# Kernel tuning notes

Hardware: AMD Instinct MI355X
Metric: run time of the kernel (lower is better)

Reference implementation:

```python
import jax, jax.numpy as jnp
import numpy as np

N_HEADS = 8
N_LAYERS = 2
LN_EPS = 1e-5


def _mha(x, Win, bin_, Wout, bout):
    # torch nn.MultiheadAttention, eval mode (dropout off). x: [b, s, d]
    b, s, d = x.shape
    dh = d // N_HEADS
    qkv = x @ Win.T + bin_                      # [b, s, 3d]
    q, k, v = jnp.split(qkv, 3, axis=-1)
    q = q.reshape(b, s, N_HEADS, dh)
    k = k.reshape(b, s, N_HEADS, dh)
    v = v.reshape(b, s, N_HEADS, dh)
    scores = jnp.einsum('bqhd,bkhd->bhqk', q, k) / jnp.sqrt(jnp.asarray(dh, x.dtype))
    attn = jax.nn.softmax(scores, axis=-1)
    o = jnp.einsum('bhqk,bkhd->bqhd', attn, v).reshape(b, s, d)
    return o @ Wout.T + bout


def _layer_norm(x, g, b):
    mu = jnp.mean(x, axis=-1, keepdims=True)
    var = jnp.mean(jnp.square(x - mu), axis=-1, keepdims=True)
    return (x - mu) * jax.lax.rsqrt(var + LN_EPS) * g + b


def _vertex_conv(feat, inc, prev, Win, bin_, Wout, bout, Wproj, ln_g, ln_b, alpha):
    # feat: [b,m,d], inc: [b,m,e]
    attn = _mha(feat, Win, bin_, Wout, bout)              # [b,m,d]
    scores = jnp.einsum('bme,bmd->bed', inc, attn)        # incidence aggregation
    w = jax.nn.softmax(scores, axis=1)                    # softmax over edges
    # fused form of einsum('bme,bmd->bmed') then einsum('bmed,bed->bed')
    edge = scores * w                                     # [b,e,d]
    edge = edge @ Wproj.T                                 # no-bias projection
    edge = _layer_norm(edge, ln_g, ln_b)
    if prev is not None:
        edge = alpha * prev + (1.0 - alpha) * edge
        edge = edge + prev
    return edge


def _edge_conv(inc, edge_feat, prev, Win, bin_, Wout, bout, Wproj, ln_g, ln_b, alpha):
    # inc: [b,m,e], edge_feat: [b,e,d]
    _ = _mha(edge_feat, Win, bin_, Wout, bout)            # attn computed, output unused downstream
    wef = jnp.einsum('bed,bme->bmd', edge_feat, inc)      # edge->node aggregation
    node = wef @ Wproj.T
    node = _layer_norm(node, ln_g, ln_b)
    if prev is not None:
        node = alpha * prev + (1.0 - alpha) * node
        node = node + prev
    return node


def setup_inputs() -> dict:
    key = jax.random.key(0)
    ks = jax.random.split(key, 8)
    b, m, e, d = 8, 1024, 1536, 256
    s = 0.02
    return {
        'features': jax.random.normal(ks[0], (b, m, d), jnp.float32),
        'inc_mat': (jax.random.uniform(ks[1], (b, m, e), jnp.float32) < 0.05).astype(jnp.float32),
        'vc_Win': jax.random.normal(ks[2], (3 * d, d), jnp.float32) * s,
        'vc_bin': jnp.zeros((3 * d,), jnp.float32),
        'vc_Wout': jax.random.normal(ks[3], (d, d), jnp.float32) * s,
        'vc_bout': jnp.zeros((d,), jnp.float32),
        'vc_Wproj': jax.random.normal(ks[4], (d, d), jnp.float32) * s,
        'vc_ln_g': jnp.ones((d,), jnp.float32),
        'vc_ln_b': jnp.zeros((d,), jnp.float32),
        'vc_alpha': jnp.asarray(0.5, jnp.float32),
        'ec_Win': jax.random.normal(ks[5], (3 * d, d), jnp.float32) * s,
        'ec_bin': jnp.zeros((3 * d,), jnp.float32),
        'ec_Wout': jax.random.normal(ks[6], (d, d), jnp.float32) * s,
        'ec_bout': jnp.zeros((d,), jnp.float32),
        'ec_Wproj': jax.random.normal(ks[7], (d, d), jnp.float32) * s,
        'ec_ln_g': jnp.ones((d,), jnp.float32),
        'ec_ln_b': jnp.zeros((d,), jnp.float32),
        'ec_alpha': jnp.asarray(0.5, jnp.float32),
    }


def reference(features, inc_mat,
              vc_Win, vc_bin, vc_Wout, vc_bout, vc_Wproj, vc_ln_g, vc_ln_b, vc_alpha,
              ec_Win, ec_bin, ec_Wout, ec_bout, ec_Wproj, ec_ln_g, ec_ln_b, ec_alpha):
    vc = (vc_Win, vc_bin, vc_Wout, vc_bout, vc_Wproj, vc_ln_g, vc_ln_b, vc_alpha)
    ec = (ec_Win, ec_bin, ec_Wout, ec_bout, ec_Wproj, ec_ln_g, ec_ln_b, ec_alpha)
    edge_feats = _vertex_conv(features, inc_mat, None, *vc)
    node_feats = _edge_conv(inc_mat, edge_feats, features, *ec)
    for _ in range(N_LAYERS):  # shared weights across layers, as in the torch module
        edge_feats = _vertex_conv(features, inc_mat, edge_feats, *vc)
        node_feats = _edge_conv(inc_mat, edge_feats, node_feats, *ec)
    return node_feats, edge_feats, inc_mat
```

## Files before the change

### kernel.cpp

```cpp
#include <hip/hip_runtime.h>
#include <stdint.h>


#define DEV static __device__ __forceinline__

typedef __attribute__((ext_vector_type(8))) short bf16x8;
typedef __attribute__((ext_vector_type(4))) float f32x4;

DEV uint16_t f2bf(float x){
  union{float f; uint32_t u;} v; v.f=x;
  uint32_t r = v.u + 0x7fffu + ((v.u>>16)&1u);
  return (uint16_t)(r>>16);
}
DEV float bf2f(uint16_t b){
  union{uint32_t u; float f;} v; v.u=((uint32_t)b)<<16; return v.f;
}

DEV uint32_t cvtpk_bf16(float lo, float hi){
  uint32_t d;
  asm("v_cvt_pk_bf16_f32 %0, %1, %2" : "=v"(d) : "v"(lo), "v"(hi));
  return d;
}

#if __has_builtin(__builtin_amdgcn_exp2f)
DEV float exp2fast(float x){ return __builtin_amdgcn_exp2f(x); }
#else
DEV float exp2fast(float x){ return __expf(x * 0.6931471805599453f); }
#endif

#if __has_builtin(__builtin_amdgcn_global_load_lds)
#define HAVE_GLL 1
#else
#define HAVE_GLL 0
#endif

DEV void load_lds16(const uint16_t* g, void* l){
#if HAVE_GLL
  __builtin_amdgcn_global_load_lds((const __attribute__((address_space(1))) uint32_t*)g,
                                   (__attribute__((address_space(3))) uint32_t*)l, 16, 0, 0);
#else
  *(bf16x8*)l = *(const bf16x8*)g;
#endif
}

__global__ __launch_bounds__(256)
void prep_cast(const float* __restrict__ feats, const float* __restrict__ win,
               const float* __restrict__ wout, const float* __restrict__ wpv,
               const float* __restrict__ wpe,
               uint16_t* __restrict__ xb, uint16_t* __restrict__ ow,
               uint16_t* __restrict__ oo, uint16_t* __restrict__ ov,
               uint16_t* __restrict__ oe){
  int i = blockIdx.x*256 + threadIdx.x;
  const float* src; uint16_t* dst; int j;
  if (i < 524288){ src=feats; dst=xb; j=i; }
  else {
    i -= 524288;
    if (i < 49152){ src=win; dst=ow; j=i; }
    else if (i < 65536){ src=wout; dst=oo; j=i-49152; }
    else if (i < 81920){ src=wpv; dst=ov; j=i-65536; }
    else { src=wpe; dst=oe; j=i-81920; }
  }
  float4 v = ((const float4*)src)[j];
  union { uint16_t u[4]; uint64_t q; } p;
  p.u[0]=f2bf(v.x); p.u[1]=f2bf(v.y); p.u[2]=f2bf(v.z); p.u[3]=f2bf(v.w);
  ((uint64_t*)dst)[j] = p.q;
}

__global__ __launch_bounds__(256, 3)
void qkv_incprep(const float* __restrict__ inc, float* __restrict__ out_inc,
                 uint16_t* __restrict__ incb, uint16_t* __restrict__ incT,
                 const uint16_t* __restrict__ A, const uint16_t* __restrict__ B,
                 uint16_t* __restrict__ Cb, const float* __restrict__ bias){
  __shared__ union {
    struct { short As[128*64]; short Bs[128*64]; } g;
    float T[32][33];
  } sm;
  const int tid = threadIdx.x;
  const int bx = blockIdx.x;

  if (bx < 384){
    const int lane = tid & 63;
    const int w = tid >> 6;
    const int wm = w & 1, wn = w >> 1;
    const int r = lane & 15, q = lane >> 4;
    const int mtile = bx & 63, ntile = bx >> 6;
    const uint16_t* Ab = A + (size_t)(mtile*128)*256;
    const uint16_t* Bb = B + (size_t)(ntile*128)*256;
    f32x4 acc[4][4];
#pragma unroll
    for (int i=0;i<4;++i)
#pragma unroll
      for (int j=0;j<4;++j) acc[i][j] = (f32x4){0.f,0.f,0.f,0.f};

    const int srow = tid >> 3;
    const int sblk = tid & 7;

    for (int kb = 0; kb < 256; kb += 64){
#pragma unroll
      for (int i=0;i<4;++i){
        int row = srow + 32*i;
        int lblk = sblk ^ (row & 7);
        load_lds16(Ab + (size_t)row*256 + kb + lblk*8, (char*)sm.g.As + i*4096 + tid*16);
      }
#pragma unroll
      for (int i=0;i<4;++i){
        int row = srow + 32*i;
        int lblk = sblk ^ (row & 7);
        load_lds16(Bb + (size_t)row*256 + kb + lblk*8, (char*)sm.g.Bs + i*4096 + tid*16);
      }
      __syncthreads();
#pragma unroll
      for (int kc=0;kc<2;++kc){
        bf16x8 af[4], bfr[4];
#pragma unroll
        for (int mt=0;mt<4;++mt){
          int m = wm*64 + mt*16 + r;
          af[mt] = *(const bf16x8*)&sm.g.As[m*64 + ((kc*4 + q) ^ (m&7))*8];
        }
#pragma unroll
        for (int nt=0;nt<4;++nt){
          int n = wn*64 + nt*16 + r;
          bfr[nt] = *(const bf16x8*)&sm.g.Bs[n*64 + ((kc*4 + q) ^ (n&7))*8];
        }
#pragma unroll
        for (int mt=0;mt<4;++mt)
#pragma unroll
          for (int nt=0;nt<4;++nt)
            acc[mt][nt] = __builtin_amdgcn_mfma_f32_16x16x32_bf16(af[mt], bfr[nt], acc[mt][nt], 0,0,0);
      }
      __syncthreads();
    }

    const int gm0 = mtile*128 + wm*64;
    const int gn0 = ntile*128 + wn*64;
#pragma unroll
    for (int mt=0;mt<4;++mt){
#pragma unroll
      for (int nt=0;nt<4;++nt){
        int gn = gn0 + nt*16 + r;
        float bv = bias[gn];
#pragma unroll
        for (int reg=0;reg<4;++reg){
          int gm = gm0 + mt*16 + q*4 + reg;
          Cb[(size_t)gm*768 + gn] = f2bf(acc[mt][nt][reg] + bv);
        }
      }
    }
  } else {
    int bxp = bx - 384;
    int x = bxp % 48;
    int t = bxp / 48;
    int y = t % 32;
    int b = t / 32;
    int c0 = x*32, r0 = y*32;
    int tx = tid & 31, ty = tid >> 5;
    size_t base = (size_t)b*1024*1536;
#pragma unroll
    for (int j=0;j<4;++j){
      int r = r0 + ty + j*8;
      size_t idx = base + (size_t)r*1536 + c0 + tx;
      float v = inc[idx];
      sm.T[ty+j*8][tx] = v;
      out_inc[idx] = v;
      incb[idx] = f2bf(v);
    }
    __syncthreads();
    size_t baseT = (size_t)b*1536*1024;
#pragma unroll
    for (int j=0;j<4;++j){
      int c = c0 + ty + j*8;
      incT[baseT + (size_t)c*1024 + r0 + tx] = f2bf(sm.T[tx][ty+j*8]);
    }
  }
}

template<int WM, int BK, int EPI>
__global__ __launch_bounds__(256, 3)
void gemm_nt(const uint16_t* __restrict__ A, const uint16_t* __restrict__ B,
             uint16_t* __restrict__ Cb, const float* __restrict__ bias,
             int M, int N, int K){
  constexpr int AROWS = WM*32;
  constexpr int UPR = BK/8;
  constexpr int RPP = 256/UPR;
  __shared__ short As[AROWS*BK];
  __shared__ short Bs[128*BK];
  const int tid = threadIdx.x;
  const int lane = tid & 63;
  const int w = tid >> 6;
  const int wm = w & 1, wn = w >> 1;
  const int r = lane & 15, q = lane >> 4;
  const uint16_t* Ab = A + (size_t)(blockIdx.x*AROWS)*K;
  const uint16_t* Bb = B + (size_t)(blockIdx.y*128)*K;
  f32x4 acc[WM][4];
#pragma unroll
  for (int i=0;i<WM;++i)
#pragma unroll
    for (int j=0;j<4;++j) acc[i][j] = (f32x4){0.f,0.f,0.f,0.f};

  const int srow = tid / UPR;
  const int sblk = tid % UPR;

  for (int kb = 0; kb < K; kb += BK){
#pragma unroll
    for (int i=0;i<AROWS/RPP;++i){
      int row = srow + RPP*i;
      int lblk = sblk ^ (row & (UPR-1));
      load_lds16(Ab + (size_t)row*K + kb + lblk*8, (char*)As + i*4096 + tid*16);
    }
#pragma unroll
    for (int i=0;i<128/RPP;++i){
      int row = srow + RPP*i;
      int lblk = sblk ^ (row & (UPR-1));
      load_lds16(Bb + (size_t)row*K + kb + lblk*8, (char*)Bs + i*4096 + tid*16);
    }
    __syncthreads();
#pragma unroll
    for (int kc=0;kc<BK/32;++kc){
      bf16x8 af[WM], bfr[4];
#pragma unroll
      for (int mt=0;mt<WM;++mt){
        int m = wm*(WM*16) + mt*16 + r;
        af[mt] = *(const bf16x8*)&As[m*BK + ((kc*4 + q) ^ (m&(UPR-1)))*8];
      }
#pragma unroll
      for (int nt=0;nt<4;++nt){
// ... 1 lines not shown
        bfr[nt] = *(const bf16x8*)&Bs[n*BK + ((kc*4 + q) ^ (n&(UPR-1)))*8];
      }
#pragma unroll
      for (int mt=0;mt<WM;++mt)
#pragma unroll
        for (int nt=0;nt<4;++nt)
          acc[mt][nt] = __builtin_amdgcn_mfma_f32_16x16x32_bf16(af[mt], bfr[nt], acc[mt][nt], 0,0,0);
    }
    __syncthreads();
  }

  const int gm0 = blockIdx.x*AROWS + wm*(WM*16);
  const int gn0 = blockIdx.y*128 + wn*64;

  if constexpr (EPI == 1){
#pragma unroll
    for (int mt=0;mt<WM;++mt){
      int gmb = gm0 + mt*16 + q*4;
      size_t bb_ = (size_t)(gmb>>10)*(256*1024);
      int mm = gmb & 1023;
#pragma unroll
      for (int nt=0;nt<4;++nt){
        int gn = gn0 + nt*16 + r;
        float bv = bias ? bias[gn] : 0.f;
        union{uint16_t u[4]; uint64_t q64;} pk;
#pragma unroll
        for (int reg=0;reg<4;++reg) pk.u[reg] = f2bf(acc[mt][nt][reg] + bv);
        *(uint64_t*)(Cb + bb_ + (size_t)gn*1024 + mm) = pk.q64;
      }
    }
  } else {
#pragma unroll
    for (int mt=0;mt<WM;++mt){
#pragma unroll
      for (int nt=0;nt<4;++nt){
        int gn = gn0 + nt*16 + r;
        float bv = bias ? bias[gn] : 0.f;
#pragma unroll
        for (int reg=0;reg<4;++reg){
          int gm = gm0 + mt*16 + q*4 + reg;
          Cb[(size_t)gm*N + gn] = f2bf(acc[mt][nt][reg] + bv);
        }
      }
    }
  }
}

__global__ __launch_bounds__(256, 4)
void gemm_score(const uint16_t* __restrict__ A,
                const uint16_t* __restrict__ B,
                float* __restrict__ part,
                uint16_t* __restrict__ VE){
  __shared__ short As[32*64];
  __shared__ short Bs[256*64];
  const int tid = threadIdx.x;
  const int lane = tid & 63;
  const int w = tid >> 6;
  const int r = lane & 15, q = lane >> 4;
  const int bx = (blockIdx.x & 7)*48 + (blockIdx.x >> 3);
  const int batch = bx / 48;
  const uint16_t* Ab = A + (size_t)bx*32*1024;
  const uint16_t* Bb = B + (size_t)batch*256*1024;

  f32x4 acc[2][4];
#pragma unroll
  for (int i=0;i<2;++i)
#pragma unroll
    for (int j=0;j<4;++j) acc[i][j] = (f32x4){0.f,0.f,0.f,0.f};

  const int srow = tid >> 3;
  const int sblk = tid & 7;

  for (int kb = 0; kb < 1024; kb += 64){
    { int lblk = sblk ^ (srow & 7);
      load_lds16(Ab + (size_t)srow*1024 + kb + lblk*8, (char*)As + tid*16); }
#pragma unroll
    for (int i=0;i<8;++i){
      int row = srow + 32*i;
      int lblk = sblk ^ (row & 7);
      load_lds16(Bb + (size_t)row*1024 + kb + lblk*8, (char*)Bs + i*4096 + tid*16);
    }
    __syncthreads();
#pragma unroll
    for (int kc=0;kc<2;++kc){
      bf16x8 af[2], bfr[4];
#pragma unroll
      for (int mt=0;mt<2;++mt){
        int m = mt*16 + r;
        af[mt] = *(const bf16x8*)&As[m*64 + ((kc*4 + q) ^ (m&7))*8];
      }
#pragma unroll
      for (int nt=0;nt<4;++nt){
        int n = w*64 + nt*16 + r;
        bfr[nt] = *(const bf16x8*)&Bs[n*64 + ((kc*4 + q) ^ (n&7))*8];
      }
#pragma unroll
      for (int mt=0;mt<2;++mt)
#pragma unroll
        for (int nt=0;nt<4;++nt)
          acc[mt][nt] = __builtin_amdgcn_mfma_f32_16x16x32_bf16(af[mt], bfr[nt], acc[mt][nt], 0,0,0);
    }
    __syncthreads();
  }

#pragma unroll
  for (int nt=0;nt<4;++nt){
    int gn = w*64 + nt*16 + r;
    float s = 0.f;
#pragma unroll
    for (int mt=0;mt<2;++mt){
#pragma unroll
      for (int reg=0;reg<4;++reg){
        float v = acc[mt][nt][reg];
        float ev = __expf(v);
        s += ev;
        int row = mt*16 + q*4 + reg;
        VE[(size_t)(bx*32 + row)*256 + gn] = f2bf(v*ev);
      }
    }
    s += __shfl_xor(s, 16);
    s += __shfl_xor(s, 32);
    if (q == 0) part[(size_t)bx*256 + gn] = s;
  }
}

__global__ __launch_bounds__(256, 4)
void gemm_ln_edge(const uint16_t* __restrict__ SB, const uint16_t* __restrict__ B,
                  const float* __restrict__ part, const float* __restrict__ g,
                  const float* __restrict__ bb, const float* __restrict__ alpha,
                  float* __restrict__ out, uint16_t* __restrict__ baset){
  __shared__ short As[32*64];
  __shared__ short Bs[256*64];
  __shared__ float lnS[4][32], lnQ[4][32];
  __shared__ float PLinv[256];
  const int tid = threadIdx.x;
  const int lane = tid & 63;
  const int w = tid >> 6;
  const int r = lane & 15, q = lane >> 4;
  const int bx = (blockIdx.x & 7)*48 + (blockIdx.x >> 3);
  const int batch = bx / 48;

  {
    float s = 0.f;
#pragma unroll
    for (int i=0;i<48;++i) s += part[((size_t)batch*48 + i)*256 + tid];
    PLinv[tid] = 1.0f / s;
  }
  __syncthreads();

  f32x4 acc[2][4];
#pragma unroll
  for (int i=0;i<2;++i)
#pragma unroll
    for (int j=0;j<4;++j) acc[i][j] = (f32x4){0.f,0.f,0.f,0.f};

  const int srow = tid >> 3;
  const int sblk = tid & 7;

  for (int kb = 0; kb < 256; kb += 64){
    {
      bf16x8 v = *(const bf16x8*)(SB + (size_t)(bx*32 + srow)*256 + kb + sblk*8);
      const float* Lp = &PLinv[kb + sblk*8];
      float xv[8];
#pragma unroll
      for (int j=0;j<8;++j) xv[j] = bf2f((uint16_t)v[j]) * Lp[j];
      union{uint32_t u[4]; bf16x8 v8;} pk;
      pk.u[0] = cvtpk_bf16(xv[0], xv[1]);
      pk.u[1] = cvtpk_bf16(xv[2], xv[3]);
      pk.u[2] = cvtpk_bf16(xv[4], xv[5]);
      pk.u[3] = cvtpk_bf16(xv[6], xv[7]);
      *(bf16x8*)&As[srow*64 + (sblk ^ (srow&7))*8] = pk.v8;
    }
#pragma unroll
    for (int i=0;i<8;++i){
      int row = srow + 32*i;
      int lblk = sblk ^ (row & 7);
      load_lds16(B + (size_t)row*256 + kb + lblk*8, (char*)Bs + i*4096 + tid*16);
    }
    __syncthreads();
#pragma unroll
    for (int kc=0;kc<2;++kc){
      bf16x8 af[2], bfr[4];
#pragma unroll
      for (int mt=0;mt<2;++mt){
        int m = mt*16 + r;
        af[mt] = *(const bf16x8*)&As[m*64 + ((kc*4 + q) ^ (m&7))*8];
      }
#pragma unroll
      for (int nt=0;nt<4;++nt){
        int n = w*64 + nt*16 + r;
        bfr[nt] = *(const bf16x8*)&Bs[n*64 + ((kc*4 + q) ^ (n&7))*8];
      }
#pragma unroll
      for (int mt=0;mt<2;++mt)
#pragma unroll
        for (int nt=0;nt<4;++nt)
          acc[mt][nt] = __builtin_amdgcn_mfma_f32_16x16x32_bf16(af[mt], bfr[nt], acc[mt][nt], 0,0,0);
    }
    __syncthreads();
  }

  float rs[2][4], rq[2][4];
#pragma unroll
  for (int mt=0;mt<2;++mt)
#pragma unroll
    for (int reg=0;reg<4;++reg){
      float s=0.f, s2=0.f;
#pragma unroll
      for (int nt=0;nt<4;++nt){
        float v = acc[mt][nt][reg];
        s += v; s2 += v*v;
      }
#pragma unroll
      for (int off=1; off<16; off<<=1){ s += __shfl_xor(s,off); s2 += __shfl_xor(s2,off); }
      rs[mt][reg]=s; rq[mt][reg]=s2;
    }
  if (r == 0){
#pragma unroll
    for (int mt=0;mt<2;++mt)
#pragma unroll
      for (int reg=0;reg<4;++reg){
        int row = mt*16 + q*4 + reg;
        lnS[w][row] = rs[mt][reg];
        lnQ[w][row] = rq[mt][reg];
      }
  }
  __syncthreads();

  const float c0 = 3.0f + alpha[0];
  float mu_[2][4], rstd_[2][4];
#pragma unroll
  for (int mt=0;mt<2;++mt)
#pragma unroll
    for (int reg=0;reg<4;++reg){
      int row = mt*16 + q*4 + reg;
      float S = lnS[0][row]+lnS[1][row]+lnS[2][row]+lnS[3][row];
      float Q = lnQ[0][row]+lnQ[1][row]+lnQ[2][row]+lnQ[3][row];
      float mu = S * (1.f/256.f);
      float var = fmaxf(Q*(1.f/256.f) - mu*mu, 0.f);
      mu_[mt][reg] = mu;
      rstd_[mt][reg] = rsqrtf(var + 1e-5f);
    }

  int e0 = (bx % 48) * 32;
#pragma unroll
  for (int mt=0;mt<2;++mt){
#pragma unroll
    for (int nt=0;nt<4;++nt){
      int gn = w*64 + nt*16 + r;
      float gv = g[gn], bv = bb[gn];
      union{uint16_t u[4]; uint64_t q64;} pk;
#pragma unroll
      for (int reg=0;reg<4;++reg){
        int row = mt*16 + q*4 + reg;
        size_t gm = (size_t)bx*32 + row;
        float o = ((acc[mt][nt][reg]-mu_[mt][reg])*rstd_[mt][reg]*gv + bv) * c0;
        pk.u[reg] = f2bf(o);
        out[gm*256 + gn] = o;
      }
      int ee = e0 + mt*16 + q*4;
      *(uint64_t*)(baset + ((size_t)batch*256 + gn)*1536 + ee) = pk.q64;
    }
  }
}

__global__ __launch_bounds__(256, 3)
void gemm_node_fused(const uint16_t* __restrict__ inc,
                     const uint16_t* __restrict__ baset,
                     const uint16_t* __restrict__ wpe,
                     const float* __restrict__ g, const float* __restrict__ bb,
                     const float* __restrict__ alpha,
                     const float* __restrict__ feats, float* __restrict__ out){
  __shared__ short Ws[256*64];
  __shared__ short As2[32*256];
  __shared__ short Is[32*64];
  const int tid = threadIdx.x;
  const int lane = tid & 63;
  const int w = tid >> 6;
  const int r = lane & 15, q = lane >> 4;
  const int bx = (blockIdx.x & 7)*32 + (blockIdx.x >> 3);
  const int batch = bx >> 5;
  const int mt0 = (bx & 31) * 32;

  const int srow = tid >> 3;
  const int sblk = tid & 7;

  const uint16_t* Bb = baset + (size_t)batch*256*1536;
  const uint16_t* Ib = inc + ((size_t)batch*1024 + mt0)*1536;

  f32x4 acc1[4][2];
#pragma unroll
  for (int i=0;i<4;++i)
#pragma unroll
    for (int j=0;j<2;++j) acc1[i][j] = (f32x4){0.f,0.f,0.f,0.f};

  for (int kb = 0; kb < 1536; kb += 64){
#pragma unroll
    for (int i=0;i<8;++i){
      int row = srow + 32*i;
      int lblk = sblk ^ (row & 7);
      load_lds16(Bb + (size_t)row*1536 + kb + lblk*8, (char*)Ws + i*4096 + tid*16);
    }
    { int lblk = sblk ^ (srow & 7);
      load_lds16(Ib + (size_t)srow*1536 + kb + lblk*8, (char*)Is + tid*16); }
    __syncthreads();
#pragma unroll
    for (int kc=0;kc<2;++kc){
      bf16x8 af[4], bfr[2];
#pragma unroll
      for (int mt=0;mt<4;++mt){
        int d = w*64 + mt*16 + r;
        af[mt] = *(const bf16x8*)&Ws[d*64 + ((kc*4 + q) ^ (d&7))*8];
      }
#pragma unroll
      for (int nt=0;nt<2;++nt){
        int m = nt*16 + r;
        bfr[nt] = *(const bf16x8*)&Is[m*64 + ((kc*4 + q) ^ (m&7))*8];
      }
#pragma unroll
      for (int mt=0;mt<4;++mt)
#pragma unroll
        for (int nt=0;nt<2;++nt)
          acc1[mt][nt] = __builtin_amdgcn_mfma_f32_16x16x32_bf16(af[mt], bfr[nt], acc1[mt][nt], 0,0,0);
    }
    __syncthreads();
  }

#pragma unroll
  for (int mt=0;mt<4;++mt){
    int j = w*8 + mt*2 + (q>>1);
#pragma unroll
    for (int nt=0;nt<2;++nt){
      int m = nt*16 + r;
      union{uint16_t u[4]; uint64_t q64;} pk;
#pragma unroll
      for (int reg=0;reg<4;++reg) pk.u[reg] = f2bf(acc1[mt][nt][reg]);
      *(uint64_t*)((char*)As2 + m*512 + ((j ^ (m&7))<<4) + ((q&1)<<3)) = pk.q64;
    }
  }

  f32x4 acc2[4][2];
#pragma unroll
  for (int i=0;i<4;++i)
#pragma unroll
    for (int j=0;j<2;++j) acc2[i][j] = (f32x4){0.f,0.f,0.f,0.f};

  for (int kb = 0; kb < 256; kb += 64){
#pragma unroll
    for (int i=0;i<8;++i){
      int row = srow + 32*i;
      int lblk = sblk ^ (row & 7);
      load_lds16(wpe + (size_t)row*256 + kb + lblk*8, (char*)Ws + i*4096 + tid*16);
    }
    __syncthreads();
#pragma unroll
    for (int kc=0;kc<2;++kc){
      bf16x8 af[4], bfr[2];
#pragma unroll
      for (int mt=0;mt<4;++mt){
        int dp = w*64 + mt*16 + r;
        af[mt] = *(const bf16x8*)&Ws[dp*64 + ((kc*4 + q) ^ (dp&7))*8];
      }
#pragma unroll
      for (int nt=0;nt<2;++nt){
        int m = nt*16 + r;
        int jr = (kb>>3) + kc*4 + q;
        bfr[nt] = *(const bf16x8*)((char*)As2 + m*512 + ((jr ^ (m&7))<<4));
      }
#pragma unroll
      for (int mt=0;mt<4;++mt)
#pragma unroll
        for (int nt=0;nt<2;++nt)
          acc2[mt][nt] = __builtin_amdgcn_mfma_f32_16x16x32_bf16(af[mt], bfr[nt], acc2[mt][nt], 0,0,0);
    }
    __syncthreads();
  }

  float* lnS = (float*)Is;
  float* lnQ = lnS + 128;
  float s_[2], q_[2];
#pragma unroll
  for (int nt=0;nt<2;++nt){
    float s=0.f, s2=0.f;
#pragma unroll
    for (int mt=0;mt<4;++mt)
#pragma unroll
      for (int reg=0;reg<4;++reg){
        float v = acc2[mt][nt][reg];
        s += v; s2 += v*v;
      }
    s += __shfl_xor(s,16); s2 += __shfl_xor(s2,16);
    s += __shfl_xor(s,32); s2 += __shfl_xor(s2,32);
    s_[nt]=s; q_[nt]=s2;
  }
  if (q == 0){
#pragma unroll
    for (int nt=0;nt<2;++nt){
      lnS[w*32 + nt*16 + r] = s_[nt];
      lnQ[w*32 + nt*16 + r] = q_[nt];
    }
  }
  __syncthreads();

  const float a = alpha[0];
  const float ap1 = 1.f + a;
  const float cn = (1.f - a)*(ap1*ap1 + ap1 + 1.f);
  const float cf = ap1*ap1*ap1;

  float mu_[2], rstd_[2];
#pragma unroll
  for (int nt=0;nt<2;++nt){
    int col = nt*16 + r;
    float S = lnS[col] + lnS[32+col] + lnS[64+col] + lnS[96+col];
    float Q = lnQ[col] + lnQ[32+col] + lnQ[64+col] + lnQ[96+col];
    float mu = S * (1.f/256.f);
    float var = fmaxf(Q*(1.f/256.f) - mu*mu, 0.f);
    mu_[nt] = mu;
    rstd_[nt] = rsqrtf(var + 1e-5f);
  }

#pragma unroll
  for (int mt=0;mt<4;++mt){
    int dp0 = w*64 + mt*16 + q*4;
    float4 gv = *(const float4*)&g[dp0];
    float4 bv = *(const float4*)&bb[dp0];
#pragma unroll
    for (int nt=0;nt<2;++nt){
      int m = nt*16 + r;
      size_t gm = (size_t)batch*1024 + mt0 + m;
      float4 fv = *(const float4*)&feats[gm*256 + dp0];
      float4 ov;
      ov.x = cf*fv.x + cn*((acc2[mt][nt][0]-mu_[nt])*rstd_[nt]*gv.x + bv.x);
      ov.y = cf*fv.y + cn*((acc2[mt][nt][1]-mu_[nt])*rstd_[nt]*gv.y + bv.y);
      ov.z = cf*fv.z + cn*((acc2[mt][nt][2]-mu_[nt])*rstd_[nt]*gv.z + bv.z);
      ov.w = cf*fv.w + cn*((acc2[mt][nt][3]-mu_[nt])*rstd_[nt]*gv.w + bv.w);
      *(float4*)&out[gm*256 + dp0] = ov;
    }
  }
}

DEV void stage_K(short* Kl, const uint16_t* __restrict__ qkv, size_t rowbase,
                 int c, int h, int kr){
  const uint16_t* kp = qkv + ((rowbase + c*256 + kr)*768 + 256 + h*32);
  int sz = (kr&3) ^ ((kr>>2)&1);
#pragma unroll
  for (int lb=0; lb<4; ++lb){
    bf16x8 v = *(const bf16x8*)(kp + lb*8);
    *(bf16x8*)&Kl[kr*32 + ((lb ^ sz))*8] = v;
  }
}

DEV void stage_V(short* VT, const uint16_t* __restrict__ qkv, size_t rowbase,
                 int c, int h, int t){
  int kvp = (t>>1)*2;
  int dhh = (t&1)*16;
  const uint16_t* v0 = qkv + ((rowbase + c*256 + kvp)*768 + 512 + h*32 + dhh);
  const uint16_t* v1 = v0 + 768;
  bf16x8 a0 = *(const bf16x8*)(v0);
  bf16x8 a1 = *(const bf16x8*)(v0+8);
  bf16x8 b0 = *(const bf16x8*)(v1);
  bf16x8 b1 = *(const bf16x8*)(v1+8);
  int blkbase = kvp>>3, off = kvp&7;
#pragma unroll
  for (int i=0;i<8;++i){
    int dh = dhh + i;
    uint32_t pack = (uint32_t)(uint16_t)a0[i] | ((uint32_t)(uint16_t)b0[i]<<16);
    *(uint32_t*)&VT[dh*256 + ((blkbase ^ (dh&7))*8) + off] = pack;
  }
#pragma unroll
  for (int i=0;i<8;++i){
    int dh = dhh + 8 + i;
    uint32_t pack = (uint32_t)(uint16_t)a1[i] | ((uint32_t)(uint16_t)b1[i]<<16);
    *(uint32_t*)&VT[dh*256 + ((blkbase ^ (dh&7))*8) + off] = pack;
  }
}

__global__ __launch_bounds__(512)
void attn_fwd(const uint16_t* __restrict__ qkv, uint16_t* __restrict__ O){
  __shared__ short Kl[256*32];
  __shared__ short VT[32*256];
  __shared__ short Pl[8][16*36];
  const int tid = threadIdx.x, lane = tid&63, w = tid>>6;
  const int r = lane&15, q = lane>>4;
  const int logical = (blockIdx.x & 7)*64 + (blockIdx.x >> 3);
  const int bh = logical >> 3, qc = logical & 7;
  const int b = bh>>3, h = bh&7;
  const int q0 = qc*128 + w*16;
  const size_t rowbase = (size_t)b*1024;

  bf16x8 aq;
// ... 37 lines not shown
        *(uint64_t*)&Pl[w][r*36 + t2*16 + q*4] = pk.q64;
      }
      bf16x8 bv[2];
#pragma unroll
      for (int db=0;db<2;++db){
        int dh = db*16 + r;
        bv[db] = *(const bf16x8*)&VT[dh*256 + (((s32*4 + q) ^ (dh&7)))*8];
      }
      bf16x8 ap = *(const bf16x8*)&Pl[w][r*36 + q*8];
      __builtin_amdgcn_s_setprio(1);
#pragma unroll
      for (int db=0;db<2;++db)
        o[db] = __builtin_amdgcn_mfma_f32_16x16x32_bf16(ap, bv[db], o[db], 0,0,0);
      __builtin_amdgcn_s_setprio(0);
    }
  }

  l += __shfl_xor(l, 16);
  l += __shfl_xor(l, 32);
#pragma unroll
  for (int db=0;db<2;++db)
#pragma unroll
    for (int reg=0;reg<4;++reg){
      float li = __shfl(l, q*4 + reg);
      int qr = q0 + q*4 + reg;
      O[(rowbase + qr)*256 + h*32 + db*16 + r] = f2bf(o[db][reg] / li);
    }
}

extern "C" void kernel_launch(void* const* d_in, const int* in_sizes, int n_in,
                              void* d_out, int out_size, void* d_ws, size_t ws_size,
                              hipStream_t stream){
  const float* features = (const float*)d_in[0];
  const float* inc      = (const float*)d_in[1];
  const float* vc_Win   = (const float*)d_in[2];
  const float* vc_bin   = (const float*)d_in[3];
  const float* vc_Wout  = (const float*)d_in[4];
  const float* vc_bout  = (const float*)d_in[5];
  const float* vc_Wproj = (const float*)d_in[6];
  const float* vc_ln_g  = (const float*)d_in[7];
  const float* vc_ln_b  = (const float*)d_in[8];
  const float* vc_alpha = (const float*)d_in[9];
  const float* ec_Wproj = (const float*)d_in[14];
  const float* ec_ln_g  = (const float*)d_in[15];
  const float* ec_ln_b  = (const float*)d_in[16];
  const float* ec_alpha = (const float*)d_in[17];

  float* out = (float*)d_out;
  float* out_node = out;
  float* out_edge = out + 2097152;
  float* out_inc  = out + 5242880;

  char* ws = (char*)d_ws;
  uint16_t* XB     = (uint16_t*)(ws + 0);
  float*    PART   = (float*)   (ws + 0);
  uint16_t* WINB   = (uint16_t*)(ws + 4194304);
  uint16_t* WOUTB  = (uint16_t*)(ws + 4587520);
  uint16_t* WPVB   = (uint16_t*)(ws + 4718592);
  uint16_t* WPEB   = (uint16_t*)(ws + 4849664);
  uint16_t* INCB   = (uint16_t*)(ws + 4988928);
  uint16_t* INCT   = (uint16_t*)(ws + 30154752);
  uint16_t* QKVB   = (uint16_t*)(ws + 55320576);
  uint16_t* SCORESB= (uint16_t*)(ws + 55320576);
  uint16_t* OB     = (uint16_t*)(ws + 67903488);
  uint16_t* ATTNT  = (uint16_t*)(ws + 72097792);
  uint16_t* BASET  = (uint16_t*)(ws + 82583552);

  prep_cast<<<2432,256,0,stream>>>(features, vc_Win, vc_Wout, vc_Wproj, ec_Wproj,
                                   XB, WINB, WOUTB, WPVB, WPEB);

  qkv_incprep<<<12672,256,0,stream>>>(inc, out_inc, INCB, INCT,
                                      XB, WINB, QKVB, vc_bin);

  attn_fwd<<<512,512,0,stream>>>(QKVB, OB);
  gemm_nt<2,128,1><<<dim3(128,2,1),256,0,stream>>>(OB, WOUTB, ATTNT, vc_bout,
                                                   8192,256,256);

  gemm_score<<<384,256,0,stream>>>(INCT, ATTNT, PART, SCORESB);

  gemm_ln_edge<<<384,256,0,stream>>>(SCORESB, WPVB, PART, vc_ln_g, vc_ln_b,
                                     vc_alpha, out_edge, BASET);

  gemm_node_fused<<<256,256,0,stream>>>(INCB, BASET, WPEB, ec_ln_g, ec_ln_b,
                                        ec_alpha, features, out_node);
}
```

Baseline: 255.9 us.

## Fuse cast prep into QKV kernel and split score/edge/node grids finer

Drops the separate prep_cast kernel. The QKV GEMM now reads fp32 features and Win directly and converts them to bf16 while staging into LDS, and the remaining weight casts run as extra blocks of the same launch. The incidence transpose blocks each handle four 32-column tiles, which cuts the block count. gemm_score, gemm_ln_edge and gemm_node_fused are retiled into smaller per-block tiles (half the d columns, or 16 rows instead of 32), doubling their grid sizes to raise occupancy across CUs. The trade-off is less reuse per block, more redundant B-tile loads, and a QKV GEMM with a smaller k-step and no asynchronous LDS loads.

```diff
diff --git a/kernel.cpp b/kernel.cpp
--- a/kernel.cpp
+++ b/kernel.cpp
@@ -43,37 +43,18 @@
 #endif
 }
 
-__global__ __launch_bounds__(256)
-void prep_cast(const float* __restrict__ feats, const float* __restrict__ win,
-               const float* __restrict__ wout, const float* __restrict__ wpv,
-               const float* __restrict__ wpe,
-               uint16_t* __restrict__ xb, uint16_t* __restrict__ ow,
-               uint16_t* __restrict__ oo, uint16_t* __restrict__ ov,
-               uint16_t* __restrict__ oe){
-  int i = blockIdx.x*256 + threadIdx.x;
-  const float* src; uint16_t* dst; int j;
-  if (i < 524288){ src=feats; dst=xb; j=i; }
-  else {
-    i -= 524288;
-    if (i < 49152){ src=win; dst=ow; j=i; }
-    else if (i < 65536){ src=wout; dst=oo; j=i-49152; }
-    else if (i < 81920){ src=wpv; dst=ov; j=i-65536; }
-    else { src=wpe; dst=oe; j=i-81920; }
-  }
-  float4 v = ((const float4*)src)[j];
-  union { uint16_t u[4]; uint64_t q; } p;
-  p.u[0]=f2bf(v.x); p.u[1]=f2bf(v.y); p.u[2]=f2bf(v.z); p.u[3]=f2bf(v.w);
-  ((uint64_t*)dst)[j] = p.q;
-}
-
 __global__ __launch_bounds__(256, 3)
-void qkv_incprep(const float* __restrict__ inc, float* __restrict__ out_inc,
-                 uint16_t* __restrict__ incb, uint16_t* __restrict__ incT,
-                 const uint16_t* __restrict__ A, const uint16_t* __restrict__ B,
-                 uint16_t* __restrict__ Cb, const float* __restrict__ bias){
+void qkv_prep(const float* __restrict__ inc, float* __restrict__ out_inc,
+              uint16_t* __restrict__ incb, uint16_t* __restrict__ incT,
+              const float* __restrict__ feats, const float* __restrict__ win,
+              const float* __restrict__ bias, uint16_t* __restrict__ qkvb,
+              const float* __restrict__ wout, const float* __restrict__ wpv,
+              const float* __restrict__ wpe,
+              uint16_t* __restrict__ ob_w, uint16_t* __restrict__ ov_w,
+              uint16_t* __restrict__ oe_w){
   __shared__ union {
-    struct { short As[128*64]; short Bs[128*64]; } g;
-    float T[32][33];
+    struct { short As[128*32]; short Bs[128*32]; } g;
+    float T[4][32][33];
   } sm;
   const int tid = threadIdx.x;
   const int bx = blockIdx.x;
@@ -84,50 +65,57 @@
     const int wm = w & 1, wn = w >> 1;
     const int r = lane & 15, q = lane >> 4;
     const int mtile = bx & 63, ntile = bx >> 6;
-    const uint16_t* Ab = A + (size_t)(mtile*128)*256;
-    const uint16_t* Bb = B + (size_t)(ntile*128)*256;
+    const float* Fb = feats + (size_t)(mtile*128)*256;
+    const float* Wb = win + (size_t)(ntile*128)*256;
     f32x4 acc[4][4];
 #pragma unroll
     for (int i=0;i<4;++i)
 #pragma unroll
       for (int j=0;j<4;++j) acc[i][j] = (f32x4){0.f,0.f,0.f,0.f};
 
-    const int srow = tid >> 3;
-    const int sblk = tid & 7;
-
-    for (int kb = 0; kb < 256; kb += 64){
-#pragma unroll
-      for (int i=0;i<4;++i){
-        int row = srow + 32*i;
-        int lblk = sblk ^ (row & 7);
-        load_lds16(Ab + (size_t)row*256 + kb + lblk*8, (char*)sm.g.As + i*4096 + tid*16);
-      }
-#pragma unroll
-      for (int i=0;i<4;++i){
-        int row = srow + 32*i;
-        int lblk = sblk ^ (row & 7);
-        load_lds16(Bb + (size_t)row*256 + kb + lblk*8, (char*)sm.g.Bs + i*4096 + tid*16);
+    const int srow = tid >> 2;
+    const int sblk = tid & 3;
+
+    for (int kb = 0; kb < 256; kb += 32){
+#pragma unroll
+      for (int i=0;i<2;++i){
+        int row = srow + 64*i;
+        const float* src = Fb + (size_t)row*256 + kb + sblk*8;
+        float4 a0 = *(const float4*)src;
+        float4 a1 = *(const float4*)(src+4);
+        union{uint32_t u[4]; bf16x8 v8;} pk;
+        pk.u[0]=cvtpk_bf16(a0.x,a0.y); pk.u[1]=cvtpk_bf16(a0.z,a0.w);
+        pk.u[2]=cvtpk_bf16(a1.x,a1.y); pk.u[3]=cvtpk_bf16(a1.z,a1.w);
+        *(bf16x8*)&sm.g.As[row*32 + (sblk ^ (row&3))*8] = pk.v8;
+      }
+#pragma unroll
+      for (int i=0;i<2;++i){
+        int row = srow + 64*i;
+        const float* src = Wb + (size_t)row*256 + kb + sblk*8;
+        float4 a0 = *(const float4*)src;
+        float4 a1 = *(const float4*)(src+4);
+        union{uint32_t u[4]; bf16x8 v8;} pk;
+        pk.u[0]=cvtpk_bf16(a0.x,a0.y); pk.u[1]=cvtpk_bf16(a0.z,a0.w);
+        pk.u[2]=cvtpk_bf16(a1.x,a1.y); pk.u[3]=cvtpk_bf16(a1.z,a1.w);
+        *(bf16x8*)&sm.g.Bs[row*32 + (sblk ^ (row&3))*8] = pk.v8;
       }
       __syncthreads();
-#pragma unroll
-      for (int kc=0;kc<2;++kc){
-        bf16x8 af[4], bfr[4];
-#pragma unroll
-        for (int mt=0;mt<4;++mt){
-          int m = wm*64 + mt*16 + r;
-          af[mt] = *(const bf16x8*)&sm.g.As[m*64 + ((kc*4 + q) ^ (m&7))*8];
-        }
-#pragma unroll
-        for (int nt=0;nt<4;++nt){
-          int n = wn*64 + nt*16 + r;
-          bfr[nt] = *(const bf16x8*)&sm.g.Bs[n*64 + ((kc*4 + q) ^ (n&7))*8];
-        }
-#pragma unroll
-        for (int mt=0;mt<4;++mt)
-#pragma unroll
-          for (int nt=0;nt<4;++nt)
-            acc[mt][nt] = __builtin_amdgcn_mfma_f32_16x16x32_bf16(af[mt], bfr[nt], acc[mt][nt], 0,0,0);
-      }
+      bf16x8 af[4], bfr[4];
+#pragma unroll
+      for (int mt=0;mt<4;++mt){
+        int m = wm*64 + mt*16 + r;
+        af[mt] = *(const bf16x8*)&sm.g.As[m*32 + (q ^ (m&3))*8];
+      }
+#pragma unroll
+      for (int nt=0;nt<4;++nt){
+        int n = wn*64 + nt*16 + r;
+        bfr[nt] = *(const bf16x8*)&sm.g.Bs[n*32 + (q ^ (n&3))*8];
+      }
+#pragma unroll
+      for (int mt=0;mt<4;++mt)
+#pragma unroll
+        for (int nt=0;nt<4;++nt)
+          acc[mt][nt] = __builtin_amdgcn_mfma_f32_16x16x32_bf16(af[mt], bfr[nt], acc[mt][nt], 0,0,0);
       __syncthreads();
     }
 
@@ -142,35 +130,53 @@
 #pragma unroll
         for (int reg=0;reg<4;++reg){
           int gm = gm0 + mt*16 + q*4 + reg;
-          Cb[(size_t)gm*768 + gn] = f2bf(acc[mt][nt][reg] + bv);
+          qkvb[(size_t)gm*768 + gn] = f2bf(acc[mt][nt][reg] + bv);
         }
       }
     }
-  } else {
-    int bxp = bx - 384;
-    int x = bxp % 48;
-    int t = bxp / 48;
+  } else if (bx < 3456){
+    int p = bx - 384;
+    int x = p % 12;
+    int t = p / 12;
     int y = t % 32;
     int b = t / 32;
-    int c0 = x*32, r0 = y*32;
+    int r0 = y*32;
     int tx = tid & 31, ty = tid >> 5;
     size_t base = (size_t)b*1024*1536;
-#pragma unroll
-    for (int j=0;j<4;++j){
-      int r = r0 + ty + j*8;
-      size_t idx = base + (size_t)r*1536 + c0 + tx;
-      float v = inc[idx];
-      sm.T[ty+j*8][tx] = v;
-      out_inc[idx] = v;
-      incb[idx] = f2bf(v);
-    }
-    __syncthreads();
     size_t baseT = (size_t)b*1536*1024;
 #pragma unroll
-    for (int j=0;j<4;++j){
-      int c = c0 + ty + j*8;
-      incT[baseT + (size_t)c*1024 + r0 + tx] = f2bf(sm.T[tx][ty+j*8]);
-    }
+    for (int s=0;s<4;++s){
+      int c0 = x*128 + s*32;
+#pragma unroll
+      for (int j=0;j<4;++j){
+        int rr = r0 + ty + j*8;
+        size_t idx = base + (size_t)rr*1536 + c0 + tx;
+        float v = inc[idx];
+        sm.T[s][ty+j*8][tx] = v;
+        out_inc[idx] = v;
+        incb[idx] = f2bf(v);
+      }
+    }
+    __syncthreads();
+#pragma unroll
+    for (int s=0;s<4;++s){
+      int c0 = x*128 + s*32;
+#pragma unroll
+      for (int j=0;j<4;++j){
+        int c = c0 + ty + j*8;
+        incT[baseT + (size_t)c*1024 + r0 + tx] = f2bf(sm.T[s][tx][ty+j*8]);
+      }
+    }
+  } else {
+    int i = (bx - 3456)*256 + tid;
+    const float* src; uint16_t* dst; int j;
+    if (i < 16384){ src=wout; dst=ob_w; j=i; }
+    else if (i < 32768){ src=wpv; dst=ov_w; j=i-16384; }
+    else { src=wpe; dst=oe_w; j=i-32768; }
+    float4 v = ((const float4*)src)[j];
+    union { uint16_t u[4]; uint64_t q; } p;
+    p.u[0]=f2bf(v.x); p.u[1]=f2bf(v.y); p.u[2]=f2bf(v.z); p.u[3]=f2bf(v.w);
+    ((uint64_t*)dst)[j] = p.q;
   }
 }
 
@@ -278,21 +284,23 @@
                 float* __restrict__ part,
                 uint16_t* __restrict__ VE){
   __shared__ short As[32*64];
-  __shared__ short Bs[256*64];
+  __shared__ short Bs[128*64];
   const int tid = threadIdx.x;
   const int lane = tid & 63;
   const int w = tid >> 6;
   const int r = lane & 15, q = lane >> 4;
-  const int bx = (blockIdx.x & 7)*48 + (blockIdx.x >> 3);
-  const int batch = bx / 48;
-  const uint16_t* Ab = A + (size_t)bx*32*1024;
-  const uint16_t* Bb = B + (size_t)batch*256*1024;
-
-  f32x4 acc[2][4];
+  const int bx = (blockIdx.x & 7)*96 + (blockIdx.x >> 3);
+  const int batch = bx / 96;
+  const int t = bx % 96;
+  const int etile = t >> 1, dh = t & 1;
+  const uint16_t* Ab = A + (size_t)(batch*1536 + etile*32)*1024;
+  const uint16_t* Bb = B + (size_t)(batch*256 + dh*128)*1024;
+
+  f32x4 acc[2][2];
 #pragma unroll
   for (int i=0;i<2;++i)
 #pragma unroll
-    for (int j=0;j<4;++j) acc[i][j] = (f32x4){0.f,0.f,0.f,0.f};
+    for (int j=0;j<2;++j) acc[i][j] = (f32x4){0.f,0.f,0.f,0.f};
 
   const int srow = tid >> 3;
   const int sblk = tid & 7;
@@ -301,7 +309,7 @@
     { int lblk = sblk ^ (srow & 7);
       load_lds16(Ab + (size_t)srow*1024 + kb + lblk*8, (char*)As + tid*16); }
 #pragma unroll
-    for (int i=0;i<8;++i){
+    for (int i=0;i<4;++i){
       int row = srow + 32*i;
       int lblk = sblk ^ (row & 7);
       load_lds16(Bb + (size_t)row*1024 + kb + lblk*8, (char*)Bs + i*4096 + tid*16);
@@ -309,29 +317,30 @@
     __syncthreads();
 #pragma unroll
     for (int kc=0;kc<2;++kc){
-      bf16x8 af[2], bfr[4];
+      bf16x8 af[2], bfr[2];
 #pragma unroll
       for (int mt=0;mt<2;++mt){
         int m = mt*16 + r;
         af[mt] = *(const bf16x8*)&As[m*64 + ((kc*4 + q) ^ (m&7))*8];
       }
 #pragma unroll
-      for (int nt=0;nt<4;++nt){
-        int n = w*64 + nt*16 + r;
+      for (int nt=0;nt<2;++nt){
+        int n = w*32 + nt*16 + r;
         bfr[nt] = *(const bf16x8*)&Bs[n*64 + ((kc*4 + q) ^ (n&7))*8];
       }
 #pragma unroll
       for (int mt=0;mt<2;++mt)
 #pragma unroll
-        for (int nt=0;nt<4;++nt)
+        for (int nt=0;nt<2;++nt)
           acc[mt][nt] = __builtin_amdgcn_mfma_f32_16x16x32_bf16(af[mt], bfr[nt], acc[mt][nt], 0,0,0);
     }
     __syncthreads();
   }
 
-#pragma unroll
-  for (int nt=0;nt<4;++nt){
-    int gn = w*64 + nt*16 + r;
+  const size_t er0 = (size_t)batch*1536 + etile*32;
+#pragma unroll
+  for (int nt=0;nt<2;++nt){
+    int gn = dh*128 + w*32 + nt*16 + r;
     float s = 0.f;
 #pragma unroll
     for (int mt=0;mt<2;++mt){
@@ -341,12 +350,12 @@
         float ev = __expf(v);
         s += ev;
         int row = mt*16 + q*4 + reg;
-        VE[(size_t)(bx*32 + row)*256 + gn] = f2bf(v*ev);
+        VE[(er0 + row)*256 + gn] = f2bf(v*ev);
       }
     }
     s += __shfl_xor(s, 16);
     s += __shfl_xor(s, 32);
-    if (q == 0) part[(size_t)bx*256 + gn] = s;
+    if (q == 0) part[(size_t)(batch*48 + etile)*256 + gn] = s;
   }
 }
 
@@ -355,16 +364,16 @@
                   const float* __restrict__ part, const float* __restrict__ g,
                   const float* __restrict__ bb, const float* __restrict__ alpha,
                   float* __restrict__ out, uint16_t* __restrict__ baset){
-  __shared__ short As[32*64];
+  __shared__ short As[16*64];
   __shared__ short Bs[256*64];
-  __shared__ float lnS[4][32], lnQ[4][32];
+  __shared__ float lnS[4][16], lnQ[4][16];
   __shared__ float PLinv[256];
   const int tid = threadIdx.x;
   const int lane = tid & 63;
   const int w = tid >> 6;
   const int r = lane & 15, q = lane >> 4;
-  const int bx = (blockIdx.x & 7)*48 + (blockIdx.x >> 3);
-  const int batch = bx / 48;
+  const int bx = (blockIdx.x & 7)*96 + (blockIdx.x >> 3);
+  const int batch = bx / 96;
 
   {
     float s = 0.f;
@@ -374,18 +383,16 @@
   }
   __syncthreads();
 
-  f32x4 acc[2][4];
-#pragma unroll
-  for (int i=0;i<2;++i)
-#pragma unroll
-    for (int j=0;j<4;++j) acc[i][j] = (f32x4){0.f,0.f,0.f,0.f};
+  f32x4 acc[4];
+#pragma unroll
+  for (int j=0;j<4;++j) acc[j] = (f32x4){0.f,0.f,0.f,0.f};
 
   const int srow = tid >> 3;
   const int sblk = tid & 7;
 
   for (int kb = 0; kb < 256; kb += 64){
-    {
-      bf16x8 v = *(const bf16x8*)(SB + (size_t)(bx*32 + srow)*256 + kb + sblk*8);
+    if (tid < 128){
+      bf16x8 v = *(const bf16x8*)(SB + (size_t)(bx*16 + srow)*256 + kb + sblk*8);
       const float* Lp = &PLinv[kb + sblk*8];
       float xv[8];
 #pragma unroll
@@ -406,87 +413,73 @@
     __syncthreads();
 #pragma unroll
     for (int kc=0;kc<2;++kc){
-      bf16x8 af[2], bfr[4];
-#pragma unroll
-      for (int mt=0;mt<2;++mt){
-        int m = mt*16 + r;
-        af[mt] = *(const bf16x8*)&As[m*64 + ((kc*4 + q) ^ (m&7))*8];
-      }
+      bf16x8 af, bfr[4];
+      { int m = r;
+        af = *(const bf16x8*)&As[m*64 + ((kc*4 + q) ^ (m&7))*8]; }
 #pragma unroll
       for (int nt=0;nt<4;++nt){
         int n = w*64 + nt*16 + r;
         bfr[nt] = *(const bf16x8*)&Bs[n*64 + ((kc*4 + q) ^ (n&7))*8];
       }
 #pragma unroll
-      for (int mt=0;mt<2;++mt)
-#pragma unroll
-        for (int nt=0;nt<4;++nt)
-          acc[mt][nt] = __builtin_amdgcn_mfma_f32_16x16x32_bf16(af[mt], bfr[nt], acc[mt][nt], 0,0,0);
-    }
-    __syncthreads();
-  }
-
-  float rs[2][4], rq[2][4];
-#pragma unroll
-  for (int mt=0;mt<2;++mt)
+      for (int nt=0;nt<4;++nt)
+        acc[nt] = __builtin_amdgcn_mfma_f32_16x16x32_bf16(af, bfr[nt], acc[nt], 0,0,0);
+    }
+    __syncthreads();
+  }
+
+  float rs[4], rq[4];
+#pragma unroll
+  for (int reg=0;reg<4;++reg){
+    float s=0.f, s2=0.f;
+#pragma unroll
+    for (int nt=0;nt<4;++nt){
+      float v = acc[nt][reg];
+      s += v; s2 += v*v;
+    }
+#pragma unroll
+    for (int off=1; off<16; off<<=1){ s += __shfl_xor(s,off); s2 += __shfl_xor(s2,off); }
+    rs[reg]=s; rq[reg]=s2;
+  }
+  if (r == 0){
 #pragma unroll
     for (int reg=0;reg<4;++reg){
-      float s=0.f, s2=0.f;
-#pragma unroll
-      for (int nt=0;nt<4;++nt){
-        float v = acc[mt][nt][reg];
-        s += v; s2 += v*v;
-      }
-#pragma unroll
-      for (int off=1; off<16; off<<=1){ s += __shfl_xor(s,off); s2 += __shfl_xor(s2,off); }
-      rs[mt][reg]=s; rq[mt][reg]=s2;
-    }
-  if (r == 0){
-#pragma unroll
-    for (int mt=0;mt<2;++mt)
-#pragma unroll
-      for (int reg=0;reg<4;++reg){
-        int row = mt*16 + q*4 + reg;
-        lnS[w][row] = rs[mt][reg];
-        lnQ[w][row] = rq[mt][reg];
-      }
+      int row = q*4 + reg;
+      lnS[w][row] = rs[reg];
+      lnQ[w][row] = rq[reg];
+    }
   }
   __syncthreads();
 
   const float c0 = 3.0f + alpha[0];
-  float mu_[2][4], rstd_[2][4];
-#pragma unroll
-  for (int mt=0;mt<2;++mt)
+  float mu_[4], rstd_[4];
+#pragma unroll
+  for (int reg=0;reg<4;++reg){
+    int row = q*4 + reg;
+    float S = lnS[0][row]+lnS[1][row]+lnS[2][row]+lnS[3][row];
+    float Q = lnQ[0][row]+lnQ[1][row]+lnQ[2][row]+lnQ[3][row];
+    float mu = S * (1.f/256.f);
+    float var = fmaxf(Q*(1.f/256.f) - mu*mu, 0.f);
+    mu_[reg] = mu;
+    rstd_[reg] = rsqrtf(var + 1e-5f);
+  }
+
+  int e0 = (bx % 96) * 16;
+#pragma unroll
+  for (int nt=0;nt<4;++nt){
+    int gn = w*64 + nt*16 + r;
+    float gv = g[gn], bv = bb[gn];
+    union{uint16_t u[4]; uint64_t q64;} pk;
 #pragma unroll
     for (int reg=0;reg<4;++reg){
-      int row = mt*16 + q*4 + reg;
-      float S = lnS[0][row]+lnS[1][row]+lnS[2][row]+lnS[3][row];
-      float Q = lnQ[0][row]+lnQ[1][row]+lnQ[2][row]+lnQ[3][row];
-      float mu = S * (1.f/256.f);
-      float var = fmaxf(Q*(1.f/256.f) - mu*mu, 0.f);
-      mu_[mt][reg] = mu;
-      rstd_[mt][reg] = rsqrtf(var + 1e-5f);
-    }
-
-  int e0 = (bx % 48) * 32;
-#pragma unroll
-  for (int mt=0;mt<2;++mt){
-#pragma unroll
-    for (int nt=0;nt<4;++nt){
-      int gn = w*64 + nt*16 + r;
-      float gv = g[gn], bv = bb[gn];
-      union{uint16_t u[4]; uint64_t q64;} pk;
-#pragma unroll
-      for (int reg=0;reg<4;++reg){
-        int row = mt*16 + q*4 + reg;
-        size_t gm = (size_t)bx*32 + row;
-        float o = ((acc[mt][nt][reg]-mu_[mt][reg])*rstd_[mt][reg]*gv + bv) * c0;
-        pk.u[reg] = f2bf(o);
-        out[gm*256 + gn] = o;
-      }
-      int ee = e0 + mt*16 + q*4;
-      *(uint64_t*)(baset + ((size_t)batch*256 + gn)*1536 + ee) = pk.q64;
-    }
+      int row = q*4 + reg;
+      size_t gm = (size_t)bx*16 + row;
+      float o = ((acc[nt][reg]-mu_[reg])*rstd_[reg]*gv + bv) * c0;
+      pk.u[reg] = f2bf(o);
+      out[gm*256 + gn] = o;
+    }
+    int ee = e0 + q*4;
+    *(uint64_t*)(baset + ((size_t)batch*256 + gn)*1536 + ee) = pk.q64;
   }
 }
 
@@ -498,15 +491,15 @@
                      const float* __restrict__ alpha,
                      const float* __restrict__ feats, float* __restrict__ out){
   __shared__ short Ws[256*64];
-  __shared__ short As2[32*256];
-  __shared__ short Is[32*64];
+  __shared__ short As2[16*256];
+  __shared__ short Is[16*64];
   const int tid = threadIdx.x;
   const int lane = tid & 63;
   const int w = tid >> 6;
   const int r = lane & 15, q = lane >> 4;
-  const int bx = (blockIdx.x & 7)*32 + (blockIdx.x >> 3);
-  const int batch = bx >> 5;
-  const int mt0 = (bx & 31) * 32;
+  const int bx = (blockIdx.x & 7)*64 + (blockIdx.x >> 3);
+  const int batch = bx >> 6;
+  const int mt0 = (bx & 63) * 16;
 
   const int srow = tid >> 3;
   const int sblk = tid & 7;
@@ -514,11 +507,9 @@
   const uint16_t* Bb = baset + (size_t)batch*256*1536;
   const uint16_t* Ib = inc + ((size_t)batch*1024 + mt0)*1536;
 
-  f32x4 acc1[4][2];
-#pragma unroll
-  for (int i=0;i<4;++i)
-#pragma unroll
-    for (int j=0;j<2;++j) acc1[i][j] = (f32x4){0.f,0.f,0.f,0.f};
+  f32x4 acc1[4];
+#pragma unroll
+  for (int i=0;i<4;++i) acc1[i] = (f32x4){0.f,0.f,0.f,0.f};
 
   for (int kb = 0; kb < 1536; kb += 64){
 #pragma unroll
@@ -527,27 +518,24 @@
       int lblk = sblk ^ (row & 7);
       load_lds16(Bb + (size_t)row*1536 + kb + lblk*8, (char*)Ws + i*4096 + tid*16);
     }
-    { int lblk = sblk ^ (srow & 7);
-      load_lds16(Ib + (size_t)srow*1536 + kb + lblk*8, (char*)Is + tid*16); }
+    if (tid < 128){
+      int lblk = sblk ^ (srow & 7);
+      load_lds16(Ib + (size_t)srow*1536 + kb + lblk*8, (char*)Is + tid*16);
+    }
     __syncthreads();
 #pragma unroll
     for (int kc=0;kc<2;++kc){
-      bf16x8 af[4], bfr[2];
+      bf16x8 af[4], bfr;
 #pragma unroll
       for (int mt=0;mt<4;++mt){
         int d = w*64 + mt*16 + r;
         af[mt] = *(const bf16x8*)&Ws[d*64 + ((kc*4 + q) ^ (d&7))*8];
       }
-#pragma unroll
-      for (int nt=0;nt<2;++nt){
-        int m = nt*16 + r;
-        bfr[nt] = *(const bf16x8*)&Is[m*64 + ((kc*4 + q) ^ (m&7))*8];
-      }
+      { int m = r;
+        bfr = *(const bf16x8*)&Is[m*64 + ((kc*4 + q) ^ (m&7))*8]; }
 #pragma unroll
       for (int mt=0;mt<4;++mt)
-#pragma unroll
-        for (int nt=0;nt<2;++nt)
-          acc1[mt][nt] = __builtin_amdgcn_mfma_f32_16x16x32_bf16(af[mt], bfr[nt], acc1[mt][nt], 0,0,0);
+        acc1[mt] = __builtin_amdgcn_mfma_f32_16x16x32_bf16(af[mt], bfr, acc1[mt], 0,0,0);
     }
     __syncthreads();
   }
@@ -555,21 +543,16 @@
 #pragma unroll
   for (int mt=0;mt<4;++mt){
     int j = w*8 + mt*2 + (q>>1);
-#pragma unroll
-    for (int nt=0;nt<2;++nt){
-      int m = nt*16 + r;
-      union{uint16_t u[4]; uint64_t q64;} pk;
-#pragma unroll
-      for (int reg=0;reg<4;++reg) pk.u[reg] = f2bf(acc1[mt][nt][reg]);
-      *(uint64_t*)((char*)As2 + m*512 + ((j ^ (m&7))<<4) + ((q&1)<<3)) = pk.q64;
-    }
-  }
-
-  f32x4 acc2[4][2];
-#pragma unroll
-  for (int i=0;i<4;++i)
-#pragma unroll
-    for (int j=0;j<2;++j) acc2[i][j] = (f32x4){0.f,0.f,0.f,0.f};
+    int m = r;
+    union{uint16_t u[4]; uint64_t q64;} pk;
+#pragma unroll
+    for (int reg=0;reg<4;++reg) pk.u[reg] = f2bf(acc1[mt][reg]);
+    *(uint64_t*)((char*)As2 + m*512 + ((j ^ (m&7))<<4) + ((q&1)<<3)) = pk.q64;
+  }
+
+  f32x4 acc2[4];
+#pragma unroll
+  for (int i=0;i<4;++i) acc2[i] = (f32x4){0.f,0.f,0.f,0.f};
 
   for (int kb = 0; kb < 256; kb += 64){
 #pragma unroll
@@ -581,50 +564,41 @@
     __syncthreads();
 #pragma unroll
     for (int kc=0;kc<2;++kc){
-      bf16x8 af[4], bfr[2];
+      bf16x8 af[4], bfr;
 #pragma unroll
       for (int mt=0;mt<4;++mt){
         int dp = w*64 + mt*16 + r;
         af[mt] = *(const bf16x8*)&Ws[dp*64 + ((kc*4 + q) ^ (dp&7))*8];
       }
-#pragma unroll
-      for (int nt=0;nt<2;++nt){
-        int m = nt*16 + r;
+      { int m = r;
         int jr = (kb>>3) + kc*4 + q;
-        bfr[nt] = *(const bf16x8*)((char*)As2 + m*512 + ((jr ^ (m&7))<<4));
-      }
+        bfr = *(const bf16x8*)((char*)As2 + m*512 + ((jr ^ (m&7))<<4)); }
 #pragma unroll
       for (int mt=0;mt<4;++mt)
-#pragma unroll
-        for (int nt=0;nt<2;++nt)
-          acc2[mt][nt] = __builtin_amdgcn_mfma_f32_16x16x32_bf16(af[mt], bfr[nt], acc2[mt][nt], 0,0,0);
+        acc2[mt] = __builtin_amdgcn_mfma_f32_16x16x32_bf16(af[mt], bfr, acc2[mt], 0,0,0);
     }
     __syncthreads();
   }
 
   float* lnS = (float*)Is;
-  float* lnQ = lnS + 128;
-  float s_[2], q_[2];
-#pragma unroll
-  for (int nt=0;nt<2;++nt){
+  float* lnQ = lnS + 64;
+  float s_, q_;
+  {
     float s=0.f, s2=0.f;
 #pragma unroll
     for (int mt=0;mt<4;++mt)
 #pragma unroll
       for (int reg=0;reg<4;++reg){
-        float v = acc2[mt][nt][reg];
+        float v = acc2[mt][reg];
         s += v; s2 += v*v;
       }
     s += __shfl_xor(s,16); s2 += __shfl_xor(s2,16);
     s += __shfl_xor(s,32); s2 += __shfl_xor(s2,32);
-    s_[nt]=s; q_[nt]=s2;
+    s_ = s; q_ = s2;
   }
   if (q == 0){
-#pragma unroll
-    for (int nt=0;nt<2;++nt){
-      lnS[w*32 + nt*16 + r] = s_[nt];
-      lnQ[w*32 + nt*16 + r] = q_[nt];
-    }
+    lnS[w*16 + r] = s_;
+    lnQ[w*16 + r] = q_;
   }
   __syncthreads();
 
@@ -633,16 +607,15 @@
   const float cn = (1.f - a)*(ap1*ap1 + ap1 + 1.f);
   const float cf = ap1*ap1*ap1;
 
-  float mu_[2], rstd_[2];
-#pragma unroll
-  for (int nt=0;nt<2;++nt){
-    int col = nt*16 + r;
-    float S = lnS[col] + lnS[32+col] + lnS[64+col] + lnS[96+col];
-    float Q = lnQ[col] + lnQ[32+col] + lnQ[64+col] + lnQ[96+col];
+  float mu_, rstd_;
+  {
+    int col = r;
+    float S = lnS[col] + lnS[16+col] + lnS[32+col] + lnS[48+col];
+    float Q = lnQ[col] + lnQ[16+col] + lnQ[32+col] + lnQ[48+col];
     float mu = S * (1.f/256.f);
     float var = fmaxf(Q*(1.f/256.f) - mu*mu, 0.f);
-    mu_[nt] = mu;
-    rstd_[nt] = rsqrtf(var + 1e-5f);
+    mu_ = mu;
+    rstd_ = rsqrtf(var + 1e-5f);
   }
 
 #pragma unroll
@@ -650,18 +623,15 @@
     int dp0 = w*64 + mt*16 + q*4;
     float4 gv = *(const float4*)&g[dp0];
     float4 bv = *(const float4*)&bb[dp0];
-#pragma unroll
-    for (int nt=0;nt<2;++nt){
-      int m = nt*16 + r;
-      size_t gm = (size_t)batch*1024 + mt0 + m;
-      float4 fv = *(const float4*)&feats[gm*256 + dp0];
-      float4 ov;
-      ov.x = cf*fv.x + cn*((acc2[mt][nt][0]-mu_[nt])*rstd_[nt]*gv.x + bv.x);
-      ov.y = cf*fv.y + cn*((acc2[mt][nt][1]-mu_[nt])*rstd_[nt]*gv.y + bv.y);
-      ov.z = cf*fv.z + cn*((acc2[mt][nt][2]-mu_[nt])*rstd_[nt]*gv.z + bv.z);
-      ov.w = cf*fv.w + cn*((acc2[mt][nt][3]-mu_[nt])*rstd_[nt]*gv.w + bv.w);
-      *(float4*)&out[gm*256 + dp0] = ov;
-    }
+    int m = r;
+    size_t gm = (size_t)batch*1024 + mt0 + m;
+    float4 fv = *(const float4*)&feats[gm*256 + dp0];
+    float4 ov;
+    ov.x = cf*fv.x + cn*((acc2[mt][0]-mu_)*rstd_*gv.x + bv.x);
+    ov.y = cf*fv.y + cn*((acc2[mt][1]-mu_)*rstd_*gv.y + bv.y);
+    ov.z = cf*fv.z + cn*((acc2[mt][2]-mu_)*rstd_*gv.z + bv.z);
+    ov.w = cf*fv.w + cn*((acc2[mt][3]-mu_)*rstd_*gv.w + bv.w);
+    *(float4*)&out[gm*256 + dp0] = ov;
   }
 }
 
@@ -805,9 +775,7 @@
   float* out_inc  = out + 5242880;
 
   char* ws = (char*)d_ws;
-  uint16_t* XB     = (uint16_t*)(ws + 0);
   float*    PART   = (float*)   (ws + 0);
-  uint16_t* WINB   = (uint16_t*)(ws + 4194304);
   uint16_t* WOUTB  = (uint16_t*)(ws + 4587520);
   uint16_t* WPVB   = (uint16_t*)(ws + 4718592);
   uint16_t* WPEB   = (uint16_t*)(ws + 4849664);
@@ -819,21 +787,20 @@
   uint16_t* ATTNT  = (uint16_t*)(ws + 72097792);
   uint16_t* BASET  = (uint16_t*)(ws + 82583552);
 
-  prep_cast<<<2432,256,0,stream>>>(features, vc_Win, vc_Wout, vc_Wproj, ec_Wproj,
-                                   XB, WINB, WOUTB, WPVB, WPEB);
-
-  qkv_incprep<<<12672,256,0,stream>>>(inc, out_inc, INCB, INCT,
-                                      XB, WINB, QKVB, vc_bin);
+  qkv_prep<<<3648,256,0,stream>>>(inc, out_inc, INCB, INCT,
+                                  features, vc_Win, vc_bin, QKVB,
+                                  vc_Wout, vc_Wproj, ec_Wproj,
+                                  WOUTB, WPVB, WPEB);
 
   attn_fwd<<<512,512,0,stream>>>(QKVB, OB);
   gemm_nt<2,128,1><<<dim3(128,2,1),256,0,stream>>>(OB, WOUTB, ATTNT, vc_bout,
                                                    8192,256,256);
 
-  gemm_score<<<384,256,0,stream>>>(INCT, ATTNT, PART, SCORESB);
-
-  gemm_ln_edge<<<384,256,0,stream>>>(SCORESB, WPVB, PART, vc_ln_g, vc_ln_b,
+  gemm_score<<<768,256,0,stream>>>(INCT, ATTNT, PART, SCORESB);
+
+  gemm_ln_edge<<<768,256,0,stream>>>(SCORESB, WPVB, PART, vc_ln_g, vc_ln_b,
                                      vc_alpha, out_edge, BASET);
 
-  gemm_node_fused<<<256,256,0,stream>>>(INCB, BASET, WPEB, ec_ln_g, ec_ln_b,
+  gemm_node_fused<<<512,256,0,stream>>>(INCB, BASET, WPEB, ec_ln_g, ec_ln_b,
                                         ec_alpha, features, out_node);
 }
```

Measured after the change: 249.5 us. 2.5% less time.
